# Kernel optimization log

Measured on AMD Instinct MI355X. Metric: run time of the kernel, lower is better.

## Reference

```python
import jax, jax.numpy as jnp
import numpy as np

CUTOFF = 5.0
NUM_RADIAL = 6
HIDDEN = 128
N_NODES = 100000
N_EDGES = 800000
MAX_Z = 95
P = 6  # envelope_exponent(5) + 1, per PyG Envelope


def _envelope(x):
    # PyG DimeNet Envelope: (1/x + a*x^(p-1) + b*x^p + c*x^(p+1)) * (x < 1)
    a = -(P + 1) * (P + 2) / 2.0   # -28
    b = P * (P + 2)                # 48
    c = -P * (P + 1) / 2.0         # -21
    xp0 = x ** (P - 1)
    xp1 = xp0 * x
    xp2 = xp1 * x
    return (1.0 / x + a * xp0 + b * xp1 + c * xp2) * (x < 1.0)


def setup_inputs():
    key = jax.random.key(0)
    ks = jax.random.split(key, 8)
    z = jax.random.randint(ks[0], (N_NODES,), 0, MAX_Z, dtype=jnp.int32)
    pos = jax.random.normal(ks[1], (N_NODES, 3), dtype=jnp.float32)
    ei = jax.random.randint(ks[2], (2, N_EDGES), 0, N_NODES, dtype=jnp.int32)
    i, j = ei[0], ei[1]
    j = jnp.where(j == i, (j + 1) % N_NODES, j)  # radius_graph emits no self-loops (avoids d=0)
    edge_index = jnp.stack([i, j])
    # BesselBasisLayer learnable frequencies: pi * n
    freq = np.pi * jnp.arange(1, NUM_RADIAL + 1, dtype=jnp.float32)
    s3 = float(np.sqrt(3.0))
    emb_table = jax.random.uniform(ks[3], (MAX_Z, HIDDEN), jnp.float32, -s3, s3)
    W_rbf = jax.random.normal(ks[4], (NUM_RADIAL, HIDDEN), jnp.float32) * (1.0 / np.sqrt(NUM_RADIAL))
    b_rbf = jnp.zeros((HIDDEN,), jnp.float32)
    W_lin = jax.random.normal(ks[5], (3 * HIDDEN, HIDDEN), jnp.float32) * (1.0 / np.sqrt(3 * HIDDEN))
    b_lin = jnp.zeros((HIDDEN,), jnp.float32)
    return {"z": z, "pos": pos, "edge_index": edge_index, "freq": freq,
            "emb_table": emb_table, "W_rbf": W_rbf, "b_rbf": b_rbf,
            "W_lin": W_lin, "b_lin": b_lin}


def reference(z, pos, edge_index, freq, emb_table, W_rbf, b_rbf, W_lin, b_lin):
    n = z.shape[0]
    i, j = edge_index[0], edge_index[1]
    # per-edge distance  [E]
    d = jnp.sqrt(jnp.sum((pos[i] - pos[j]) ** 2, axis=-1))
    # Bessel RBF  [E, num_radial]
    x = d[:, None] / CUTOFF
    rbf = _envelope(x) * jnp.sin(freq * x)
    # DimeNet EmbeddingBlock (act = SiLU/swish)
    h_rbf = jax.nn.silu(rbf @ W_rbf + b_rbf)            # [E, H]
    xz = emb_table[z]                                    # [N, H]
    e_emb = jax.nn.silu(
        jnp.concatenate([xz[i], xz[j], h_rbf], axis=-1) @ W_lin + b_lin
    )                                                    # [E, H]
    # scatter_mean over target node j -> [N, H]
    sums = jax.ops.segment_sum(e_emb, j, num_segments=n)
    cnt = jax.ops.segment_sum(jnp.ones_like(d), j, num_segments=n)
    v_emb = sums / jnp.maximum(cnt, 1.0)[:, None]
    return v_emb  # pool=None -> node-level embeddings
```

## Files before the change

kernel.cpp:

```cpp
#include <hip/hip_runtime.h>
#include <hip/hip_bf16.h>
#include <math.h>

#define HID 128
#define NRAD 6
#define TABN 4096
#define CUTOFF_INV 0.2f
#define MZ 95
#define PAD 32
#define OVF_CAP 65536

typedef unsigned int uint32;

__global__ void build1(const float* __restrict__ emb, const float* __restrict__ W_lin,
                       const float* __restrict__ freq, const float* __restrict__ W_rbf,
                       const float* __restrict__ b_rbf, const float* __restrict__ b_lin,
                       const int* __restrict__ ei, const float* __restrict__ pos,
                       const int* __restrict__ z,
                       __hip_bfloat16* __restrict__ Tb, float* __restrict__ ftab,
                       int* __restrict__ cnt, int* __restrict__ payload,
                       int* __restrict__ ovfcnt, int2* __restrict__ ovfbuf,
                       int MAXZ, int E) {
    __shared__ float sh[HID];
    int h   = threadIdx.x;
    int bid = blockIdx.x;
    int nT  = 2 * MAXZ;
    int nF  = TABN + 1;
    if (bid < nT) {
        int zz = bid >> 1, s = bid & 1;
        sh[h] = emb[zz * HID + h];
        __syncthreads();
        const float* W = W_lin + (size_t)s * HID * HID;
        float acc = (s == 0) ? b_lin[h] : 0.f;
#pragma unroll 8
        for (int k = 0; k < HID; ++k) acc = fmaf(sh[k], W[k * HID + h], acc);
        Tb[(size_t)(s * MAXZ + zz) * HID + h] = __float2bfloat16(acc);
    } else if (bid < nT + nF) {
        int t = bid - nT;
        float rbf[NRAD];
        if (t == 0) {
#pragma unroll
            for (int k = 0; k < NRAD; ++k) rbf[k] = freq[k];
        } else if (t >= TABN) {
#pragma unroll
            for (int k = 0; k < NRAD; ++k) rbf[k] = 0.f;
        } else {
            float x  = (float)t / (float)TABN;
            float x2 = x * x, x5 = x2 * x2 * x;
            float env = 1.f / x + x5 * (-28.f + x * (48.f + x * (-21.f)));
#pragma unroll
            for (int k = 0; k < NRAD; ++k) rbf[k] = env * sinf(freq[k] * x);
        }
        float pre = b_rbf[h];
#pragma unroll
        for (int k = 0; k < NRAD; ++k) pre = fmaf(rbf[k], W_rbf[k * HID + h], pre);
        sh[h] = pre / (1.f + __expf(-pre));
        __syncthreads();
        const float* W3 = W_lin + (size_t)2 * HID * HID;
        float acc = 0.f;
#pragma unroll 8
        for (int k = 0; k < HID; ++k) acc = fmaf(sh[k], W3[k * HID + h], acc);
        ftab[(size_t)t * HID + h] = acc;
    } else {
        int e = (bid - nT - nF) * HID + h;
        if (e < E) {
            int i = ei[e];
            int j = ei[E + e];
            float dx = pos[3 * i]     - pos[3 * j];
            float dy = pos[3 * i + 1] - pos[3 * j + 1];
            float dz = pos[3 * i + 2] - pos[3 * j + 2];
            float d  = sqrtf(dx * dx + dy * dy + dz * dz);
            float u  = fminf(d * CUTOFF_INV, 1.0f) * (float)TABN;
            int   ti = (int)(u + 0.5f);
            if (ti > TABN) ti = TABN;
            int pl = ti | (z[i] << 13) | (z[j] << 20);
            int r  = atomicAdd(&cnt[j], 1);
            if (r < PAD) {
                payload[j * PAD + r] = pl;
            } else {
                int o = atomicAdd(ovfcnt, 1);
                if (o < OVF_CAP) ovfbuf[o] = make_int2(j, pl);
            }
        }
    }
}

__launch_bounds__(1024)
__global__ void gather_k(const int* __restrict__ cnt, const int* __restrict__ payload,
                         const uint32* __restrict__ Tb32, const float* __restrict__ ftab,
                         float* __restrict__ out, int N) {
    __shared__ uint32 sT[2 * MZ * (HID / 2)];
    int tid = threadIdx.x;
    for (int k = tid; k < 2 * MZ * (HID / 2); k += 1024) sT[k] = Tb32[k];
    __syncthreads();

    int lane = tid & 63, wv = tid >> 6;
    int h2   = lane * 2;
    const uint32* sT2 = sT + MZ * (HID / 2);
    const float*  ft  = ftab + h2;
    int nCh = (N + 15) >> 4;

    for (int ch = blockIdx.x; ch < nCh; ch += gridDim.x) {
        int n = (ch << 4) + wv;
        if (n >= N) continue;
        int deg = cnt[n];
        int cb  = deg < PAD ? deg : PAD;
        int plv = payload[n * PAD + (lane & (PAD - 1))];

        float a0 = 0.f, a1 = 0.f;
        for (int k = 0; k < cb; ++k) {
            int pl = __builtin_amdgcn_readlane(plv, k);
            int ti = pl & 0x1FFF;
            int zi = (pl >> 13) & 0x7F;
            int zj = (pl >> 20) & 0x7F;
            float2 f  = *(const float2*)(ft + (size_t)ti * HID);
            uint32 u1 = sT[zi * (HID / 2) + lane];
            uint32 u2 = sT2[zj * (HID / 2) + lane];
            float p0 = __uint_as_float(u1 << 16)         + __uint_as_float(u2 << 16)         + f.x;
            float p1 = __uint_as_float(u1 & 0xFFFF0000u) + __uint_as_float(u2 & 0xFFFF0000u) + f.y;
            a0 = fmaf(p0, __builtin_amdgcn_rcpf(1.f + __expf(-p0)), a0);
            a1 = fmaf(p1, __builtin_amdgcn_rcpf(1.f + __expf(-p1)), a1);
        }
        float s = (deg > 0) ? 1.0f / (float)deg : 0.0f;
        float2 o; o.x = a0 * s; o.y = a1 * s;
        *(float2*)(out + (size_t)n * HID + h2) = o;
    }
}

__global__ void fixup_k(const int* __restrict__ ovfcnt, const int2* __restrict__ ovfbuf,
                        const int* __restrict__ cnt, const uint32* __restrict__ Tb32,
                        const float* __restrict__ ftab, float* __restrict__ out, int MAXZ) {
    int nov = *ovfcnt;
    if (nov > OVF_CAP) nov = OVF_CAP;
    int total = nov * 64;
    int stride = gridDim.x * blockDim.x;
    const uint32* T2b = Tb32 + MAXZ * (HID / 2);
    for (int u = blockIdx.x * blockDim.x + threadIdx.x; u < total; u += stride) {
        int ent = u >> 6, lane = u & 63;
        int2 v = ovfbuf[ent];
        int j  = v.x, pl = v.y;
        int ti = pl & 0x1FFF;
        int zi = (pl >> 13) & 0x7F;
        int zj = (pl >> 20) & 0x7F;
        float2 f  = *(const float2*)(ftab + (size_t)ti * HID + lane * 2);
        uint32 u1 = Tb32[zi * (HID / 2) + lane];
        uint32 u2 = T2b[zj * (HID / 2) + lane];
        float p0 = __uint_as_float(u1 << 16)         + __uint_as_float(u2 << 16)         + f.x;
        float p1 = __uint_as_float(u1 & 0xFFFF0000u) + __uint_as_float(u2 & 0xFFFF0000u) + f.y;
        float s  = 1.0f / (float)max(cnt[j], 1);
        atomicAdd(&out[(size_t)j * HID + lane * 2],     p0 * __builtin_amdgcn_rcpf(1.f + __expf(-p0)) * s);
        atomicAdd(&out[(size_t)j * HID + lane * 2 + 1], p1 * __builtin_amdgcn_rcpf(1.f + __expf(-p1)) * s);
    }
}

extern "C" void kernel_launch(void* const* d_in, const int* in_sizes, int n_in,
                              void* d_out, int out_size, void* d_ws, size_t ws_size,
                              hipStream_t stream) {
    const int*   z     = (const int*)d_in[0];
    const float* pos   = (const float*)d_in[1];
    const int*   ei    = (const int*)d_in[2];
    const float* freq  = (const float*)d_in[3];
    const float* emb   = (const float*)d_in[4];
    const float* W_rbf = (const float*)d_in[5];
    const float* b_rbf = (const float*)d_in[6];
    const float* W_lin = (const float*)d_in[7];
    const float* b_lin = (const float*)d_in[8];

    int N    = in_sizes[0];
    int E    = in_sizes[2] / 2;
    int MAXZ = in_sizes[4] / HID;
    float* out = (float*)d_out;

    int N_pad = ((N + 1024) / 1024) * 1024;

    char* ws = (char*)d_ws;
    size_t off = 0;
    auto alloc = [&](size_t bytes) { char* p = ws + off; off = (off + bytes + 255) & ~(size_t)255; return p; };
    int*   cnt     = (int*)alloc((size_t)N_pad * 4);
    int*   ovfcnt  = (int*)alloc(256);
    __hip_bfloat16* Tb = (__hip_bfloat16*)alloc((size_t)2 * MAXZ * HID * 2);
    float* ftab    = (float*)alloc((size_t)(TABN + 1) * HID * 4);
    int*   payload = (int*)alloc((size_t)N_pad * PAD * 4);
    int2*  ovfbuf  = (int2*)alloc((size_t)OVF_CAP * 8);

    hipMemsetAsync(cnt, 0, (size_t)N_pad * 4 + 256, stream);

    int nBuild = 2 * MAXZ + (TABN + 1) + (E + HID - 1) / HID;
    build1<<<nBuild, HID, 0, stream>>>(emb, W_lin, freq, W_rbf, b_rbf, b_lin,
                                       ei, pos, z, Tb, ftab, cnt, payload,
                                       ovfcnt, ovfbuf, MAXZ, E);
    gather_k<<<512, 1024, 0, stream>>>(cnt, payload, (const uint32*)Tb, ftab, out, N);
    fixup_k<<<128, 256, 0, stream>>>(ovfcnt, ovfbuf, cnt, (const uint32*)Tb, ftab, out, MAXZ);
}
```

Baseline: 190.9 us.

## Fold overflow fixup into gather, use half-wave per node, shrink table and padding

The gather kernel now gives each node a 32-lane group, with each lane handling four features, and splits edges across two accumulator sets. Nodes whose degree exceeds the smaller padding of 16 scan the global overflow buffer themselves, so the separate atomic fixup kernel is gone. The per-slot padding is halved to shrink payload traffic, and the distance lookup table is halved to cut build-kernel work. The trade-offs are a coarser RBF table, which costs accuracy, more overflow entries, and a linear overflow scan for each high-degree node.

```diff
diff --git a/kernel.cpp b/kernel.cpp
--- a/kernel.cpp
+++ b/kernel.cpp
@@ -4,10 +4,10 @@
 
 #define HID 128
 #define NRAD 6
-#define TABN 4096
+#define TABN 2048
 #define CUTOFF_INV 0.2f
 #define MZ 95
-#define PAD 32
+#define PAD 16
 #define OVF_CAP 65536
 
 typedef unsigned int uint32;
@@ -88,68 +88,66 @@
 __launch_bounds__(1024)
 __global__ void gather_k(const int* __restrict__ cnt, const int* __restrict__ payload,
                          const uint32* __restrict__ Tb32, const float* __restrict__ ftab,
+                         const int* __restrict__ ovfcnt, const int2* __restrict__ ovfbuf,
                          float* __restrict__ out, int N) {
     __shared__ uint32 sT[2 * MZ * (HID / 2)];
     int tid = threadIdx.x;
     for (int k = tid; k < 2 * MZ * (HID / 2); k += 1024) sT[k] = Tb32[k];
     __syncthreads();
 
-    int lane = tid & 63, wv = tid >> 6;
-    int h2   = lane * 2;
+    int lane = tid & 31, grp = tid >> 5;
+    int h4   = lane * 4;
     const uint32* sT2 = sT + MZ * (HID / 2);
-    const float*  ft  = ftab + h2;
-    int nCh = (N + 15) >> 4;
+    const float*  ft  = ftab + h4;
+    int nCh = (N + 31) >> 5;
 
     for (int ch = blockIdx.x; ch < nCh; ch += gridDim.x) {
-        int n = (ch << 4) + wv;
+        int n = (ch << 5) + grp;
         if (n >= N) continue;
         int deg = cnt[n];
         int cb  = deg < PAD ? deg : PAD;
         int plv = payload[n * PAD + (lane & (PAD - 1))];
 
-        float a0 = 0.f, a1 = 0.f;
-        for (int k = 0; k < cb; ++k) {
-            int pl = __builtin_amdgcn_readlane(plv, k);
+        float e0 = 0.f, e1 = 0.f, e2 = 0.f, e3 = 0.f;
+        float o0 = 0.f, o1 = 0.f, o2 = 0.f, o3 = 0.f;
+        auto edge = [&](int pl, float& b0, float& b1, float& b2, float& b3) {
             int ti = pl & 0x1FFF;
             int zi = (pl >> 13) & 0x7F;
             int zj = (pl >> 20) & 0x7F;
-            float2 f  = *(const float2*)(ft + (size_t)ti * HID);
-            uint32 u1 = sT[zi * (HID / 2) + lane];
-            uint32 u2 = sT2[zj * (HID / 2) + lane];
-            float p0 = __uint_as_float(u1 << 16)         + __uint_as_float(u2 << 16)         + f.x;
-            float p1 = __uint_as_float(u1 & 0xFFFF0000u) + __uint_as_float(u2 & 0xFFFF0000u) + f.y;
-            a0 = fmaf(p0, __builtin_amdgcn_rcpf(1.f + __expf(-p0)), a0);
-            a1 = fmaf(p1, __builtin_amdgcn_rcpf(1.f + __expf(-p1)), a1);
+            float4 f  = *(const float4*)(ft + (size_t)ti * HID);
+            uint2  u1 = *(const uint2*)(sT  + zi * (HID / 2) + lane * 2);
+            uint2  u2 = *(const uint2*)(sT2 + zj * (HID / 2) + lane * 2);
+            float p0 = __uint_as_float(u1.x << 16)         + __uint_as_float(u2.x << 16)         + f.x;
+            float p1 = __uint_as_float(u1.x & 0xFFFF0000u) + __uint_as_float(u2.x & 0xFFFF0000u) + f.y;
+            float p2 = __uint_as_float(u1.y << 16)         + __uint_as_float(u2.y << 16)         + f.z;
+            float p3 = __uint_as_float(u1.y & 0xFFFF0000u) + __uint_as_float(u2.y & 0xFFFF0000u) + f.w;
+            b0 = fmaf(p0, __builtin_amdgcn_rcpf(1.f + __expf(-p0)), b0);
+            b1 = fmaf(p1, __builtin_amdgcn_rcpf(1.f + __expf(-p1)), b1);
+            b2 = fmaf(p2, __builtin_amdgcn_rcpf(1.f + __expf(-p2)), b2);
+            b3 = fmaf(p3, __builtin_amdgcn_rcpf(1.f + __expf(-p3)), b3);
+        };
+        int k = 0;
+        for (; k + 2 <= cb; k += 2) {
+            int plA = __shfl(plv, k, 32);
+            int plB = __shfl(plv, k + 1, 32);
+            edge(plA, e0, e1, e2, e3);
+            edge(plB, o0, o1, o2, o3);
+        }
+        if (k < cb) { int plA = __shfl(plv, k, 32); edge(plA, e0, e1, e2, e3); }
+
+        if (deg > PAD) {
+            int nov = *ovfcnt;
+            if (nov > OVF_CAP) nov = OVF_CAP;
+            for (int o = 0; o < nov; ++o) {
+                int2 v = ovfbuf[o];
+                if (v.x == n) edge(v.y, e0, e1, e2, e3);
+            }
         }
         float s = (deg > 0) ? 1.0f / (float)deg : 0.0f;
-        float2 o; o.x = a0 * s; o.y = a1 * s;
-        *(float2*)(out + (size_t)n * HID + h2) = o;
-    }
-}
-
-__global__ void fixup_k(const int* __restrict__ ovfcnt, const int2* __restrict__ ovfbuf,
-                        const int* __restrict__ cnt, const uint32* __restrict__ Tb32,
-                        const float* __restrict__ ftab, float* __restrict__ out, int MAXZ) {
-    int nov = *ovfcnt;
-    if (nov > OVF_CAP) nov = OVF_CAP;
-    int total = nov * 64;
-    int stride = gridDim.x * blockDim.x;
-    const uint32* T2b = Tb32 + MAXZ * (HID / 2);
-    for (int u = blockIdx.x * blockDim.x + threadIdx.x; u < total; u += stride) {
-        int ent = u >> 6, lane = u & 63;
-        int2 v = ovfbuf[ent];
-        int j  = v.x, pl = v.y;
-        int ti = pl & 0x1FFF;
-        int zi = (pl >> 13) & 0x7F;
-        int zj = (pl >> 20) & 0x7F;
-        float2 f  = *(const float2*)(ftab + (size_t)ti * HID + lane * 2);
-        uint32 u1 = Tb32[zi * (HID / 2) + lane];
-        uint32 u2 = T2b[zj * (HID / 2) + lane];
-        float p0 = __uint_as_float(u1 << 16)         + __uint_as_float(u2 << 16)         + f.x;
-        float p1 = __uint_as_float(u1 & 0xFFFF0000u) + __uint_as_float(u2 & 0xFFFF0000u) + f.y;
-        float s  = 1.0f / (float)max(cnt[j], 1);
-        atomicAdd(&out[(size_t)j * HID + lane * 2],     p0 * __builtin_amdgcn_rcpf(1.f + __expf(-p0)) * s);
-        atomicAdd(&out[(size_t)j * HID + lane * 2 + 1], p1 * __builtin_amdgcn_rcpf(1.f + __expf(-p1)) * s);
+        float4 v;
+        v.x = (e0 + o0) * s; v.y = (e1 + o1) * s;
+        v.z = (e2 + o2) * s; v.w = (e3 + o3) * s;
+        *(float4*)(out + (size_t)n * HID + h4) = v;
     }
 }
 
@@ -189,6 +187,6 @@
     build1<<<nBuild, HID, 0, stream>>>(emb, W_lin, freq, W_rbf, b_rbf, b_lin,
                                        ei, pos, z, Tb, ftab, cnt, payload,
                                        ovfcnt, ovfbuf, MAXZ, E);
-    gather_k<<<512, 1024, 0, stream>>>(cnt, payload, (const uint32*)Tb, ftab, out, N);
-    fixup_k<<<128, 256, 0, stream>>>(ovfcnt, ovfbuf, cnt, (const uint32*)Tb, ftab, out, MAXZ);
+    gather_k<<<512, 1024, 0, stream>>>(cnt, payload, (const uint32*)Tb, ftab,
+                                       ovfcnt, ovfbuf, out, N);
 }
```

Result: slower. 248.4 us (+30.1%).

## Bucket edge scatter by destination range, shrink tables, fold overflow into gather

Applied to the files above, without the earlier changes.

Edge scattering now runs as eight passes over the edges, each handling only destinations in one contiguous node range. This localises the atomics and payload writes, and each thread reads four j indices with one vector load. The RBF table is halved and the per-node payload slots drop from 32 to 16. The separate fixup kernel is removed: nodes with more than 16 edges scan the whole overflow buffer inside the gather kernel. This saves a launch and its atomics, but every edge index is read eight times, table resolution is coarser, and high-degree nodes (likely with mean degree 8 and PAD 16) pay a linear scan of the overflow list.

```diff
diff --git a/kernel.cpp b/kernel.cpp
--- a/kernel.cpp
+++ b/kernel.cpp
@@ -4,10 +4,10 @@
 
 #define HID 128
 #define NRAD 6
-#define TABN 4096
+#define TABN 2048
 #define CUTOFF_INV 0.2f
 #define MZ 95
-#define PAD 32
+#define PAD 16
 #define OVF_CAP 65536
 
 typedef unsigned int uint32;
@@ -20,7 +20,7 @@
                        __hip_bfloat16* __restrict__ Tb, float* __restrict__ ftab,
                        int* __restrict__ cnt, int* __restrict__ payload,
                        int* __restrict__ ovfcnt, int2* __restrict__ ovfbuf,
-                       int MAXZ, int E) {
+                       int MAXZ, int E, int bsh) {
     __shared__ float sh[HID];
     int h   = threadIdx.x;
     int bid = blockIdx.x;
@@ -62,10 +62,12 @@
         for (int k = 0; k < HID; ++k) acc = fmaf(sh[k], W3[k * HID + h], acc);
         ftab[(size_t)t * HID + h] = acc;
     } else {
-        int e = (bid - nT - nF) * HID + h;
-        if (e < E) {
-            int i = ei[e];
-            int j = ei[E + e];
+        int t = bid - nT - nF;
+        int bucket = t & 7;
+        const int* ej = ei + E;
+        auto one = [&](int e, int j) {
+            if ((j >> bsh) != bucket) return;
+            int i  = ei[e];
             float dx = pos[3 * i]     - pos[3 * j];
             float dy = pos[3 * i + 1] - pos[3 * j + 1];
             float dz = pos[3 * i + 2] - pos[3 * j + 2];
@@ -81,6 +83,14 @@
                 int o = atomicAdd(ovfcnt, 1);
                 if (o < OVF_CAP) ovfbuf[o] = make_int2(j, pl);
             }
+        };
+        int e0 = ((t >> 3) * HID + h) * 4;
+        if (e0 + 3 < E) {
+            int4 jv = *(const int4*)(ej + e0);
+            one(e0,     jv.x); one(e0 + 1, jv.y);
+            one(e0 + 2, jv.z); one(e0 + 3, jv.w);
+        } else {
+            for (int e = e0; e < E; ++e) one(e, ej[e]);
         }
     }
 }
@@ -88,6 +98,7 @@
 __launch_bounds__(1024)
 __global__ void gather_k(const int* __restrict__ cnt, const int* __restrict__ payload,
                          const uint32* __restrict__ Tb32, const float* __restrict__ ftab,
+                         const int* __restrict__ ovfcnt, const int2* __restrict__ ovfbuf,
                          float* __restrict__ out, int N) {
     __shared__ uint32 sT[2 * MZ * (HID / 2)];
     int tid = threadIdx.x;
@@ -108,8 +119,7 @@
         int plv = payload[n * PAD + (lane & (PAD - 1))];
 
         float a0 = 0.f, a1 = 0.f;
-        for (int k = 0; k < cb; ++k) {
-            int pl = __builtin_amdgcn_readlane(plv, k);
+        auto edge = [&](int pl) {
             int ti = pl & 0x1FFF;
             int zi = (pl >> 13) & 0x7F;
             int zj = (pl >> 20) & 0x7F;
@@ -120,36 +130,21 @@
             float p1 = __uint_as_float(u1 & 0xFFFF0000u) + __uint_as_float(u2 & 0xFFFF0000u) + f.y;
             a0 = fmaf(p0, __builtin_amdgcn_rcpf(1.f + __expf(-p0)), a0);
             a1 = fmaf(p1, __builtin_amdgcn_rcpf(1.f + __expf(-p1)), a1);
+        };
+        for (int k = 0; k < cb; ++k)
+            edge(__builtin_amdgcn_readlane(plv, k));
+
+        if (deg > PAD) {
+            int nov = *ovfcnt;
+            if (nov > OVF_CAP) nov = OVF_CAP;
+            for (int o = 0; o < nov; ++o) {
+                int2 v = ovfbuf[o];
+                if (v.x == n) edge(v.y);
+            }
         }
         float s = (deg > 0) ? 1.0f / (float)deg : 0.0f;
         float2 o; o.x = a0 * s; o.y = a1 * s;
         *(float2*)(out + (size_t)n * HID + h2) = o;
-    }
-}
-
-__global__ void fixup_k(const int* __restrict__ ovfcnt, const int2* __restrict__ ovfbuf,
-                        const int* __restrict__ cnt, const uint32* __restrict__ Tb32,
-                        const float* __restrict__ ftab, float* __restrict__ out, int MAXZ) {
-    int nov = *ovfcnt;
-    if (nov > OVF_CAP) nov = OVF_CAP;
-    int total = nov * 64;
-    int stride = gridDim.x * blockDim.x;
-    const uint32* T2b = Tb32 + MAXZ * (HID / 2);
-    for (int u = blockIdx.x * blockDim.x + threadIdx.x; u < total; u += stride) {
-        int ent = u >> 6, lane = u & 63;
-        int2 v = ovfbuf[ent];
-        int j  = v.x, pl = v.y;
-        int ti = pl & 0x1FFF;
-        int zi = (pl >> 13) & 0x7F;
-        int zj = (pl >> 20) & 0x7F;
-        float2 f  = *(const float2*)(ftab + (size_t)ti * HID + lane * 2);
-        uint32 u1 = Tb32[zi * (HID / 2) + lane];
-        uint32 u2 = T2b[zj * (HID / 2) + lane];
-        float p0 = __uint_as_float(u1 << 16)         + __uint_as_float(u2 << 16)         + f.x;
-        float p1 = __uint_as_float(u1 & 0xFFFF0000u) + __uint_as_float(u2 & 0xFFFF0000u) + f.y;
-        float s  = 1.0f / (float)max(cnt[j], 1);
-        atomicAdd(&out[(size_t)j * HID + lane * 2],     p0 * __builtin_amdgcn_rcpf(1.f + __expf(-p0)) * s);
-        atomicAdd(&out[(size_t)j * HID + lane * 2 + 1], p1 * __builtin_amdgcn_rcpf(1.f + __expf(-p1)) * s);
     }
 }
 
@@ -172,6 +167,8 @@
     float* out = (float*)d_out;
 
     int N_pad = ((N + 1024) / 1024) * 1024;
+    int bsh = 0;
+    while ((8 << bsh) < N) ++bsh;
 
     char* ws = (char*)d_ws;
     size_t off = 0;
@@ -185,10 +182,11 @@
 
     hipMemsetAsync(cnt, 0, (size_t)N_pad * 4 + 256, stream);
 
-    int nBuild = 2 * MAXZ + (TABN + 1) + (E + HID - 1) / HID;
+    int nQuadBlocks = (E + HID * 4 - 1) / (HID * 4);
+    int nBuild = 2 * MAXZ + (TABN + 1) + 8 * nQuadBlocks;
     build1<<<nBuild, HID, 0, stream>>>(emb, W_lin, freq, W_rbf, b_rbf, b_lin,
                                        ei, pos, z, Tb, ftab, cnt, payload,
-                                       ovfcnt, ovfbuf, MAXZ, E);
-    gather_k<<<512, 1024, 0, stream>>>(cnt, payload, (const uint32*)Tb, ftab, out, N);
-    fixup_k<<<128, 256, 0, stream>>>(ovfcnt, ovfbuf, cnt, (const uint32*)Tb, ftab, out, MAXZ);
+                                       ovfcnt, ovfbuf, MAXZ, E, bsh);
+    gather_k<<<512, 1024, 0, stream>>>(cnt, payload, (const uint32*)Tb, ftab,
+                                       ovfcnt, ovfbuf, out, N);
 }
```

Measured after the change: 260.6 us. 1.37x slower.
